# Optimization experiments

Hardware: AMD Instinct MI355X
Metric: run time of the kernel (lower is better)

## Reference

```python
import jax, jax.numpy as jnp
import numpy as np

D = 1024
H = 16
HD = D // H  # 64
FF = 4 * D
EPS = 1e-5

def _layernorm(x, g, b):
    mu = jnp.mean(x, axis=-1, keepdims=True)
    var = jnp.mean((x - mu) ** 2, axis=-1, keepdims=True)
    return (x - mu) * jax.lax.rsqrt(var + EPS) * g + b

def _apply_rotary(x, cos, sin):
    # x: [B,H,T,HD]; cos/sin: [T,HD//2] broadcast over B,H
    d = x.shape[-1] // 2
    x1, x2 = x[..., :d], x[..., d:]
    return jnp.concatenate([x1 * cos - x2 * sin, x2 * cos + x1 * sin], axis=-1)

def setup_inputs() -> dict:
    key = jax.random.key(0)
    ks = jax.random.split(key, 12)
    B, T = 4, 2048
    s = 0.02
    return {
        "x": jax.random.normal(ks[0], (B, T, D), jnp.float32),
        "rope_cos": jax.random.uniform(ks[1], (T, HD // 2), jnp.float32),
        "rope_sin": jax.random.uniform(ks[2], (T, HD // 2), jnp.float32),
        "ln1_g": jnp.ones((D,), jnp.float32),
        "ln1_b": jnp.zeros((D,), jnp.float32),
        "Wqkv": jax.random.normal(ks[3], (D, 3 * D), jnp.float32) * s,
        "bqkv": jnp.zeros((3 * D,), jnp.float32),
        "Wo": jax.random.normal(ks[4], (D, D), jnp.float32) * s,
        "bo": jnp.zeros((D,), jnp.float32),
        "ln2_g": jnp.ones((D,), jnp.float32),
        "ln2_b": jnp.zeros((D,), jnp.float32),
        "W1": jax.random.normal(ks[5], (D, FF), jnp.float32) * s,
        "b1": jnp.zeros((FF,), jnp.float32),
        "W2": jax.random.normal(ks[6], (FF, D), jnp.float32) * s,
        "b2": jnp.zeros((D,), jnp.float32),
    }

def reference(x, rope_cos, rope_sin, ln1_g, ln1_b, Wqkv, bqkv, Wo, bo, ln2_g, ln2_b, W1, b1, W2, b2):
    B, T, _ = x.shape
    h = _layernorm(x, ln1_g, ln1_b)
    qkv = (h @ Wqkv + bqkv).reshape(B, T, 3, H, HD)
    qkv = jnp.transpose(qkv, (2, 0, 3, 1, 4))  # [3,B,H,T,HD]
    q, k, v = qkv[0], qkv[1], qkv[2]
    q = _apply_rotary(q, rope_cos, rope_sin)
    k = _apply_rotary(k, rope_cos, rope_sin)
    scale = 1.0 / jnp.sqrt(jnp.float32(HD))
    scores = jnp.einsum('bhqd,bhkd->bhqk', q, k) * scale
    probs = jax.nn.softmax(scores, axis=-1)
    attn = jnp.einsum('bhqk,bhkd->bhqd', probs, v)
    attn = jnp.transpose(attn, (0, 2, 1, 3)).reshape(B, T, D)
    x = x + attn @ Wo + bo
    h2 = _layernorm(x, ln2_g, ln2_b)
    mlp = jax.nn.gelu(h2 @ W1 + b1, approximate=False) @ W2 + b2
    return x + mlp
```

## Files before the change

kernel.cpp:

```cpp
#include <hip/hip_runtime.h>
#include <hip/hip_bf16.h>
#include <math.h>

typedef __bf16 bf16x8 __attribute__((ext_vector_type(8)));
typedef float f32x4 __attribute__((ext_vector_type(4)));
typedef float f32x16 __attribute__((ext_vector_type(16)));
typedef unsigned short u16x8 __attribute__((ext_vector_type(8)));
typedef unsigned short u16x4 __attribute__((ext_vector_type(4)));
typedef unsigned int u32x4 __attribute__((ext_vector_type(4)));

#define DEV __device__ __forceinline__

DEV unsigned short f2bf(float f) { __bf16 h = (__bf16)f; return __builtin_bit_cast(unsigned short, h); }
DEV float bf2f(unsigned short u) { __bf16 h = __builtin_bit_cast(__bf16, u); return (float)h; }
DEV unsigned int pk2(float a, float b) {
  return (unsigned int)f2bf(a) | ((unsigned int)f2bf(b) << 16);
}

DEV void async_cp16(const void* g, void* l) {
  __builtin_amdgcn_global_load_lds((const __attribute__((address_space(1))) void*)g,
                                   (__attribute__((address_space(3))) void*)l, 16, 0, 0);
}

__global__ __launch_bounds__(256) void ln_kernel(const float* __restrict__ in,
    const float* __restrict__ g, const float* __restrict__ b,
    unsigned short* __restrict__ out)
{
  const int row = blockIdx.x;
  const int tid = threadIdx.x;
  const float4 v = ((const float4*)(in + (size_t)row * 1024))[tid];
  float s  = v.x + v.y + v.z + v.w;
  float sq = v.x*v.x + v.y*v.y + v.z*v.z + v.w*v.w;
  for (int m = 1; m < 64; m <<= 1) { s += __shfl_xor(s, m); sq += __shfl_xor(sq, m); }
  __shared__ float red[8];
  const int wave = tid >> 6;
  if ((tid & 63) == 0) { red[wave] = s; red[4 + wave] = sq; }
  __syncthreads();
  s  = red[0] + red[1] + red[2] + red[3];
  sq = red[4] + red[5] + red[6] + red[7];
  const float mu = s * (1.0f / 1024.0f);
  const float var = sq * (1.0f / 1024.0f) - mu * mu;
  const float rs = rsqrtf(var + 1e-5f);
  const float4 gv = ((const float4*)g)[tid];
  const float4 bv = ((const float4*)b)[tid];
  u16x4 o;
  o[0] = f2bf((v.x - mu) * rs * gv.x + bv.x);
  o[1] = f2bf((v.y - mu) * rs * gv.y + bv.y);
  o[2] = f2bf((v.z - mu) * rs * gv.z + bv.z);
  o[3] = f2bf((v.w - mu) * rs * gv.w + bv.w);
  *(u16x4*)(out + (size_t)row * 1024 + tid * 4) = o;
}

__global__ __launch_bounds__(256) void wtrans_kernel(const float* __restrict__ in,
    unsigned short* __restrict__ out, int K, int N)
{
  __shared__ float tile[32][33];
  const int n0 = blockIdx.x * 32, k0 = blockIdx.y * 32;
  const int r = threadIdx.x >> 5, c = threadIdx.x & 31;
  for (int p = 0; p < 4; ++p)
    tile[r + p * 8][c] = in[(size_t)(k0 + r + p * 8) * N + n0 + c];
  __syncthreads();
  for (int p = 0; p < 4; ++p)
    out[(size_t)(n0 + r + p * 8) * K + k0 + c] = f2bf(tile[c][r + p * 8]);
}

enum { EPI_QKV = 0, EPI_ATTNO = 1, EPI_GELU = 2, EPI_FINAL = 3 };

template <int EPI>
__global__ __launch_bounds__(256, 3) void gemm_bt(
    const unsigned short* __restrict__ A,
    const unsigned short* __restrict__ Bt,
    const float* __restrict__ bias,
    const float* __restrict__ resid,
    void* __restrict__ out,
    int M, int N, int K,
    const float* __restrict__ rc, const float* __restrict__ rsn,
    unsigned short* __restrict__ vout)
{
  __shared__ unsigned short lA[4096] __attribute__((aligned(16)));
  __shared__ unsigned short lB[4096] __attribute__((aligned(16)));
  const int tid = threadIdx.x;
  const int lane = tid & 63, wave = tid >> 6;
  const int l15 = lane & 15, quad = lane >> 4;
  const int bm = blockIdx.y * 128, bn = blockIdx.x * 128;
  const int wm = (wave & 1) * 64, wn = (wave >> 1) * 64;

  const unsigned short* ga[2]; const unsigned short* gb[2];
  unsigned short* la_dst[2]; unsigned short* lb_dst[2];
  for (int it = 0; it < 2; ++it) {
    const int s = it * 256 + tid;
    const int gg = s >> 3;
    const int v = (s & 7) ^ (gg & 7);
    const int row = gg * 2 + (v >> 2);
    const int ch = v & 3;
    ga[it] = A  + (size_t)(bm + row) * K + ch * 8;
    gb[it] = Bt + (size_t)(bn + row) * K + ch * 8;
    const int base = (it * 256 + wave * 64) * 8;
    la_dst[it] = lA + base;
    lb_dst[it] = lB + base;
  }
  int offA[4], offB[4];
  for (int i = 0; i < 4; ++i) {
    int row = wm + i * 16 + l15;
    int gg = row >> 1;
    int si = (((row & 1) << 2) | quad) ^ (gg & 7);
    offA[i] = ((gg << 3) | si) * 8;
    row = wn + i * 16 + l15;
    gg = row >> 1;
    si = (((row & 1) << 2) | quad) ^ (gg & 7);
    offB[i] = ((gg << 3) | si) * 8;
  }

  f32x4 acc[4][4];
  for (int i = 0; i < 4; ++i)
    for (int j = 0; j < 4; ++j)
      acc[i][j] = f32x4{0.f, 0.f, 0.f, 0.f};

  for (int k0 = 0; k0 < K; k0 += 32) {
    async_cp16(ga[0], la_dst[0]);
    async_cp16(ga[1], la_dst[1]);
    async_cp16(gb[0], lb_dst[0]);
    async_cp16(gb[1], lb_dst[1]);
    ga[0] += 32; ga[1] += 32; gb[0] += 32; gb[1] += 32;
    __syncthreads();
    bf16x8 af[4], bfr[4];
    for (int i = 0; i < 4; ++i) af[i]  = *(const bf16x8*)(lA + offA[i]);
    for (int j = 0; j < 4; ++j) bfr[j] = *(const bf16x8*)(lB + offB[j]);
    for (int i = 0; i < 4; ++i)
      for (int j = 0; j < 4; ++j)
        acc[i][j] = __builtin_amdgcn_mfma_f32_16x16x32_bf16(af[i], bfr[j], acc[i][j], 0, 0, 0);
    __syncthreads();
  }

  float bvals[4];
  for (int j = 0; j < 4; ++j) bvals[j] = bias[bn + wn + j * 16 + l15];

  if constexpr (EPI == EPI_QKV) {
    const int cn = bn + wn;
    const int sec = cn >> 10;
    if (sec == 2) {
      const int b = bm >> 11;
      const int hh = (cn & 1023) >> 6;
      for (int i = 0; i < 4; ++i) {
        const int t0 = (bm + wm + i * 16 + quad * 4) & 2047;
        for (int j = 0; j < 4; ++j) {
          const int d = j * 16 + l15;
          u16x4 o;
          for (int r = 0; r < 4; ++r) o[r] = f2bf(acc[i][j][r] + bvals[j]);
          *(u16x4*)(vout + ((size_t)((b * 16 + hh) * 64 + d)) * 2048 + t0) = o;
        }
      }
    } else {
      const float qscale = (sec == 0) ? 0.18033688f : 1.0f;
      unsigned short* qkvout = (unsigned short*)out;
      for (int i = 0; i < 4; ++i) {
        for (int r = 0; r < 4; ++r) {
          const int row = bm + wm + i * 16 + quad * 4 + r;
          const int t = row & 2047;
          for (int j = 0; j < 2; ++j) {
            const int d = j * 16 + l15;
            const float v1 = acc[i][j][r] + bvals[j];
            const float v2 = acc[i][j + 2][r] + bvals[j + 2];
            const float c = rc[t * 32 + d], s = rsn[t * 32 + d];
            const float o1 = (v1 * c - v2 * s) * qscale;
            const float o2 = (v2 * c + v1 * s) * qscale;
            const size_t base = (size_t)row * 3072 + cn + d;
            qkvout[base] = f2bf(o1);
            qkvout[base + 32] = f2bf(o2);
          }
        }
      }
    }
  } else {
    for (int i = 0; i < 4; ++i) {
      for (int r = 0; r < 4; ++r) {
        const size_t row = bm + wm + i * 16 + quad * 4 + r;
        for (int j = 0; j < 4; ++j) {
          const size_t col = bn + wn + j * 16 + l15;
          const float v = acc[i][j][r] + bvals[j];
          const size_t idx = row * (size_t)N + col;
          if constexpr (EPI == EPI_ATTNO) {
            ((float*)out)[idx] = resid[idx] + v;
          } else if constexpr (EPI == EPI_GELU) {
            const float gl = 0.5f * v * (1.0f + erff(v * 0.70710678118f));
            ((unsigned short*)out)[idx] = f2bf(gl);
          } else {
            ((float*)out)[idx] = resid[idx] + v;
          }
        }
      }
    }
  }
}

__global__ __launch_bounds__(256, 4) void attn_kernel(
    const unsigned short* __restrict__ qkv,
    const unsigned short* __restrict__ vt,
    unsigned short* __restrict__ outb)
{
  __shared__ unsigned short Ks[2][4096] __attribute__((aligned(16)));
  __shared__ unsigned short Vs[2][4096] __attribute__((aligned(16)));
  __shared__ float Sred[128];

  const int tid = threadIdx.x;
  const int lane = tid & 63, wave = tid >> 6;
  const int l31 = lane & 31, hl = lane >> 5;
  const int bh = blockIdx.y, b = bh >> 4, h = bh & 15;
  const int q0 = blockIdx.x * 64;
  const int qsub = (wave & 1) * 32;
  const int ksub = (wave >> 1) * 32;

  bf16x8 qf[4];
  {
    const unsigned short* qp = qkv + (size_t)(b * 2048 + q0 + qsub + l31) * 3072 + h * 64 + hl * 8;
    for (int kc = 0; kc < 4; ++kc) qf[kc] = *(const bf16x8*)(qp + kc * 16);
  }

  const int s0 = wave * 128 + lane, s1 = s0 + 64;
  const int r0 = s0 >> 3, c0 = (lane & 7) ^ (r0 & 7);
  const int r1 = s1 >> 3, c1 = (lane & 7) ^ (r1 & 7);
  const unsigned short* kbase = qkv + (size_t)(b * 2048) * 3072 + 1024 + h * 64;
  const unsigned short* ks0 = kbase + (size_t)r0 * 3072 + c0 * 8;
  const unsigned short* ks1 = kbase + (size_t)r1 * 3072 + c1 * 8;
  const unsigned short* vbase = vt + (size_t)bh * 64 * 2048;
  const unsigned short* vs0 = vbase + (size_t)r0 * 2048 + c0 * 8;
  const unsigned short* vs1 = vbase + (size_t)r1 * 2048 + c1 * 8;
  unsigned short* kd[2] = { Ks[0] + wave * 1024, Ks[1] + wave * 1024 };
  unsigned short* vd[2] = { Vs[0] + wave * 1024, Vs[1] + wave * 1024 };

  int offK[4], offV[2][2];
  for (int kc = 0; kc < 4; ++kc) {
    const int rk = ksub + l31;
    offK[kc] = (rk * 8 + ((2 * kc + hl) ^ (rk & 7))) * 8;
  }
  for (int dn = 0; dn < 2; ++dn)
    for (int c = 0; c < 2; ++c) {
      const int rv = dn * 32 + l31;
      const int ch = (ksub >> 3) + 2 * c + hl;
      offV[dn][c] = (rv * 8 + (ch ^ (rv & 7))) * 8;
    }

  f32x16 accO[2];
  for (int dn = 0; dn < 2; ++dn)
    for (int i = 0; i < 16; ++i) accO[dn][i] = 0.f;
  float rsum = 0.f;

  async_cp16(ks0, kd[0]);
  async_cp16(ks1, kd[0] + 512);
  async_cp16(vs0, vd[0]);
  async_cp16(vs1, vd[0] + 512);

  for (int kt = 0; kt < 32; ++kt) {
    const int cur = kt & 1, nxt = cur ^ 1;
    __syncthreads();
    if (kt < 31) {
      const size_t ko = (size_t)(kt + 1) * 64 * 3072;
      const int vo = (kt + 1) * 64;
      async_cp16(ks0 + ko, kd[nxt]);
      async_cp16(ks1 + ko, kd[nxt] + 512);
      async_cp16(vs0 + vo, vd[nxt]);
      async_cp16(vs1 + vo, vd[nxt] + 512);
    }
    f32x16 accS;
    for (int i = 0; i < 16; ++i) accS[i] = 0.f;
    for (int kc = 0; kc < 4; ++kc) {
      const bf16x8 kf = *(const bf16x8*)(Ks[cur] + offK[kc]);
      accS = __builtin_amdgcn_mfma_f32_32x32x16_bf16(kf, qf[kc], accS, 0, 0, 0);
    }
    float p[16];
    for (int i = 0; i < 16; ++i) {
      p[i] = __builtin_amdgcn_exp2f(accS[i]);
      rsum += p[i];
    }

    for (int c = 0; c < 2; ++c) {
      const unsigned int xlo0 = pk2(p[8 * c + 0], p[8 * c + 1]);
      const unsigned int xlo1 = pk2(p[8 * c + 2], p[8 * c + 3]);
      const unsigned int xhi0 = pk2(p[8 * c + 4], p[8 * c + 5]);
      const unsigned int xhi1 = pk2(p[8 * c + 6], p[8 * c + 7]);
      const unsigned int recv0 = __shfl_xor((int)(hl ? xlo0 : xhi0), 32);
      const unsigned int recv1 = __shfl_xor((int)(hl ? xlo1 : xhi1), 32);
      u32x4 w;
      w[0] = hl ? recv0 : xlo0;
      w[1] = hl ? recv1 : xlo1;
      w[2] = hl ? xhi0 : recv0;
      w[3] = hl ? xhi1 : recv1;
      const bf16x8 pf = __builtin_bit_cast(bf16x8, w);
      for (int dn = 0; dn < 2; ++dn) {
        const bf16x8 vf = *(const bf16x8*)(Vs[cur] + offV[dn][c]);
        accO[dn] = __builtin_amdgcn_mfma_f32_32x32x16_bf16(pf, vf, accO[dn], 0, 0, 0);
      }
    }
  }

  __syncthreads();
  float* Obuf = (float*)&Ks[0][0];

  {
    const float rs2 = rsum + __shfl_xor(rsum, 32);
    if (hl == 0) Sred[(wave >> 1) * 64 + qsub + l31] = rs2;
  }
  if (ksub == 0) {
    for (int dn = 0; dn < 2; ++dn)
      for (int reg = 0; reg < 16; ++reg) {
        const int rq = qsub + (reg & 3) + 8 * (reg >> 2) + 4 * hl;
        Obuf[rq * 64 + dn * 32 + l31] = accO[dn][reg];
      }
  }
  __syncthreads();
  if (ksub == 32) {
    for (int reg = 0; reg < 16; ++reg) {
      const int rq = qsub + (reg & 3) + 8 * (reg >> 2) + 4 * hl;
      const float inv = 1.0f / (Sred[rq] + Sred[64 + rq]);
      const size_t row = (size_t)(b * 2048 + q0 + rq);
      for (int dn = 0; dn < 2; ++dn) {
        const float o = (Obuf[rq * 64 + dn * 32 + l31] + accO[dn][reg]) * inv;
        outb[row * 1024 + h * 64 + dn * 32 + l31] = f2bf(o);
      }
    }
  }
}

extern "C" void kernel_launch(void* const* d_in, const int* in_sizes, int n_in,
                              void* d_out, int out_size, void* d_ws, size_t ws_size,
                              hipStream_t stream)
{
  const float* x        = (const float*)d_in[0];
  const float* rope_cos = (const float*)d_in[1];
  const float* rope_sin = (const float*)d_in[2];
  const float* ln1_g    = (const float*)d_in[3];
  const float* ln1_b    = (const float*)d_in[4];
  const float* Wqkv     = (const float*)d_in[5];
  const float* bqkv     = (const float*)d_in[6];
  const float* Wo       = (const float*)d_in[7];
  const float* bo       = (const float*)d_in[8];
  const float* ln2_g    = (const float*)d_in[9];
  const float* ln2_b    = (const float*)d_in[10];
  const float* W1       = (const float*)d_in[11];
  const float* b1       = (const float*)d_in[12];
  const float* W2       = (const float*)d_in[13];
  const float* b2       = (const float*)d_in[14];
  float* outp = (float*)d_out;

  char* ws = (char*)d_ws;
  size_t off = 0;
  auto alloc = [&](size_t bytes) -> void* {
    void* p = ws + off;
    off += (bytes + 255) & ~(size_t)255;
    return p;
  };
  unsigned short* h1    = (unsigned short*)alloc(8192ull * 1024 * 2);
  unsigned short* wqkvT = (unsigned short*)alloc(3072ull * 1024 * 2);
  unsigned short* woT   = (unsigned short*)alloc(1024ull * 1024 * 2);
  unsigned short* w1T   = (unsigned short*)alloc(4096ull * 1024 * 2);
  unsigned short* w2T   = (unsigned short*)alloc(1024ull * 4096 * 2);
  unsigned short* qkv   = (unsigned short*)alloc(8192ull * 3072 * 2);
  unsigned short* vtb   = (unsigned short*)alloc(64ull * 64 * 2048 * 2);
  unsigned short* h2    = (unsigned short*)alloc(8192ull * 1024 * 2);
  unsigned short* ffb   = (unsigned short*)alloc(8192ull * 4096 * 2);

  wtrans_kernel<<<dim3(96, 32), 256, 0, stream>>>(Wqkv, wqkvT, 1024, 3072);
  wtrans_kernel<<<dim3(32, 32), 256, 0, stream>>>(Wo, woT, 1024, 1024);
  wtrans_kernel<<<dim3(128, 32), 256, 0, stream>>>(W1, w1T, 1024, 4096);
  wtrans_kernel<<<dim3(32, 128), 256, 0, stream>>>(W2, w2T, 4096, 1024);

  ln_kernel<<<8192, 256, 0, stream>>>(x, ln1_g, ln1_b, h1);
  gemm_bt<EPI_QKV><<<dim3(24, 64), 256, 0, stream>>>(h1, wqkvT, bqkv, nullptr, qkv,
                                                     8192, 3072, 1024, rope_cos, rope_sin, vtb);
  attn_kernel<<<dim3(32, 64), 256, 0, stream>>>(qkv, vtb, h1);
  gemm_bt<EPI_ATTNO><<<dim3(8, 64), 256, 0, stream>>>(h1, woT, bo, x, d_out,
                                                      8192, 1024, 1024, nullptr, nullptr, nullptr);
  ln_kernel<<<8192, 256, 0, stream>>>(outp, ln2_g, ln2_b, h2);
  gemm_bt<EPI_GELU><<<dim3(32, 64), 256, 0, stream>>>(h2, w1T, b1, nullptr, ffb,
                                                      8192, 4096, 1024, nullptr, nullptr, nullptr);
  gemm_bt<EPI_FINAL><<<dim3(8, 64), 256, 0, stream>>>(ffb, w2T, b2, outp, d_out,
                                                      8192, 1024, 4096, nullptr, nullptr, nullptr);
}
```

Measured before the change: 577.9 us.

## Deepen GEMM K-tile to 64 and give each attention wave its own query rows

The GEMM kernel now stages a 64-wide K slice per iteration with a simpler per-row XOR swizzle, halving the number of barrier pairs per K loop at the cost of doubling LDS per block. The attention kernel switches from splitting keys across wave pairs to having each of four waves own 32 query rows and process all 64 keys per tile. This removes the cross-wave partial-output reduction through LDS and doubles K/V tile reuse per block, but it halves the grid size and raises per-wave work, which may reduce occupancy and parallelism.

Result: faster. 522.3 us (-9.6%).

```diff
diff --git a/kernel.cpp b/kernel.cpp
--- a/kernel.cpp
+++ b/kernel.cpp
@@ -77,58 +77,53 @@
     const float* __restrict__ rc, const float* __restrict__ rsn,
     unsigned short* __restrict__ vout)
 {
-  __shared__ unsigned short lA[4096] __attribute__((aligned(16)));
-  __shared__ unsigned short lB[4096] __attribute__((aligned(16)));
+  __shared__ unsigned short lA[8192] __attribute__((aligned(16)));
+  __shared__ unsigned short lB[8192] __attribute__((aligned(16)));
   const int tid = threadIdx.x;
   const int lane = tid & 63, wave = tid >> 6;
   const int l15 = lane & 15, quad = lane >> 4;
   const int bm = blockIdx.y * 128, bn = blockIdx.x * 128;
   const int wm = (wave & 1) * 64, wn = (wave >> 1) * 64;
 
-  const unsigned short* ga[2]; const unsigned short* gb[2];
-  unsigned short* la_dst[2]; unsigned short* lb_dst[2];
-  for (int it = 0; it < 2; ++it) {
+  const unsigned short* ga[4]; const unsigned short* gb[4];
+  unsigned short* la_dst[4]; unsigned short* lb_dst[4];
+  for (int it = 0; it < 4; ++it) {
     const int s = it * 256 + tid;
-    const int gg = s >> 3;
-    const int v = (s & 7) ^ (gg & 7);
-    const int row = gg * 2 + (v >> 2);
-    const int ch = v & 3;
+    const int row = s >> 3;
+    const int ch = (s & 7) ^ (row & 7);
     ga[it] = A  + (size_t)(bm + row) * K + ch * 8;
     gb[it] = Bt + (size_t)(bn + row) * K + ch * 8;
     const int base = (it * 256 + wave * 64) * 8;
     la_dst[it] = lA + base;
     lb_dst[it] = lB + base;
   }
-  int offA[4], offB[4];
-  for (int i = 0; i < 4; ++i) {
-    int row = wm + i * 16 + l15;
-    int gg = row >> 1;
-    int si = (((row & 1) << 2) | quad) ^ (gg & 7);
-    offA[i] = ((gg << 3) | si) * 8;
-    row = wn + i * 16 + l15;
-    gg = row >> 1;
-    si = (((row & 1) << 2) | quad) ^ (gg & 7);
-    offB[i] = ((gg << 3) | si) * 8;
-  }
+  int offA[2][4], offB[2][4];
+  for (int ks = 0; ks < 2; ++ks)
+    for (int i = 0; i < 4; ++i) {
+      int row = wm + i * 16 + l15;
+      offA[ks][i] = (row * 8 + ((ks * 4 + quad) ^ (row & 7))) * 8;
+      row = wn + i * 16 + l15;
+      offB[ks][i] = (row * 8 + ((ks * 4 + quad) ^ (row & 7))) * 8;
+    }
 
   f32x4 acc[4][4];
   for (int i = 0; i < 4; ++i)
     for (int j = 0; j < 4; ++j)
       acc[i][j] = f32x4{0.f, 0.f, 0.f, 0.f};
 
-  for (int k0 = 0; k0 < K; k0 += 32) {
-    async_cp16(ga[0], la_dst[0]);
-    async_cp16(ga[1], la_dst[1]);
-    async_cp16(gb[0], lb_dst[0]);
-    async_cp16(gb[1], lb_dst[1]);
-    ga[0] += 32; ga[1] += 32; gb[0] += 32; gb[1] += 32;
+  for (int k0 = 0; k0 < K; k0 += 64) {
+    for (int it = 0; it < 4; ++it) async_cp16(ga[it], la_dst[it]);
+    for (int it = 0; it < 4; ++it) async_cp16(gb[it], lb_dst[it]);
+    for (int it = 0; it < 4; ++it) { ga[it] += 64; gb[it] += 64; }
     __syncthreads();
-    bf16x8 af[4], bfr[4];
-    for (int i = 0; i < 4; ++i) af[i]  = *(const bf16x8*)(lA + offA[i]);
-    for (int j = 0; j < 4; ++j) bfr[j] = *(const bf16x8*)(lB + offB[j]);
-    for (int i = 0; i < 4; ++i)
-      for (int j = 0; j < 4; ++j)
-        acc[i][j] = __builtin_amdgcn_mfma_f32_16x16x32_bf16(af[i], bfr[j], acc[i][j], 0, 0, 0);
+    for (int ks = 0; ks < 2; ++ks) {
+      bf16x8 af[4], bfr[4];
+      for (int i = 0; i < 4; ++i) af[i]  = *(const bf16x8*)(lA + offA[ks][i]);
+      for (int j = 0; j < 4; ++j) bfr[j] = *(const bf16x8*)(lB + offB[ks][j]);
+      for (int i = 0; i < 4; ++i)
+        for (int j = 0; j < 4; ++j)
+          acc[i][j] = __builtin_amdgcn_mfma_f32_16x16x32_bf16(af[i], bfr[j], acc[i][j], 0, 0, 0);
+    }
     __syncthreads();
   }
 
@@ -206,9 +201,8 @@
   const int lane = tid & 63, wave = tid >> 6;
   const int l31 = lane & 31, hl = lane >> 5;
   const int bh = blockIdx.y, b = bh >> 4, h = bh & 15;
-  const int q0 = blockIdx.x * 64;
-  const int qsub = (wave & 1) * 32;
-  const int ksub = (wave >> 1) * 32;
+  const int q0 = blockIdx.x * 128;
+  const int qsub = wave * 32;
 
   bf16x8 qf[4];
   {
@@ -228,16 +222,16 @@
   unsigned short* kd[2] = { Ks[0] + wave * 1024, Ks[1] + wave * 1024 };
   unsigned short* vd[2] = { Vs[0] + wave * 1024, Vs[1] + wave * 1024 };
 
-  int offK[4], offV[2][2];
-  for (int kc = 0; kc < 4; ++kc) {
-    const int rk = ksub + l31;
-    offK[kc] = (rk * 8 + ((2 * kc + hl) ^ (rk & 7))) * 8;
-  }
+  int offK[2][4], offV[2][4];
+  for (int g = 0; g < 2; ++g)
+    for (int kc = 0; kc < 4; ++kc) {
+      const int rk = g * 32 + l31;
+      offK[g][kc] = (rk * 8 + ((2 * kc + hl) ^ (rk & 7))) * 8;
+    }
   for (int dn = 0; dn < 2; ++dn)
-    for (int c = 0; c < 2; ++c) {
+    for (int t = 0; t < 4; ++t) {
       const int rv = dn * 32 + l31;
-      const int ch = (ksub >> 3) + 2 * c + hl;
-      offV[dn][c] = (rv * 8 + (ch ^ (rv & 7))) * 8;
+      offV[dn][t] = (rv * 8 + ((2 * t + hl) ^ (rv & 7))) * 8;
     }
 
   f32x16 accO[2];
@@ -261,63 +255,51 @@
       async_cp16(vs0 + vo, vd[nxt]);
       async_cp16(vs1 + vo, vd[nxt] + 512);
     }
-    f32x16 accS;
-    for (int i = 0; i < 16; ++i) accS[i] = 0.f;
-    for (int kc = 0; kc < 4; ++kc) {
-      const bf16x8 kf = *(const bf16x8*)(Ks[cur] + offK[kc]);
-      accS = __builtin_amdgcn_mfma_f32_32x32x16_bf16(kf, qf[kc], accS, 0, 0, 0);
-    }
-    float p[16];
-    for (int i = 0; i < 16; ++i) {
-      p[i] = __builtin_amdgcn_exp2f(accS[i]);
-      rsum += p[i];
-    }
-
-    for (int c = 0; c < 2; ++c) {
-      const unsigned int xlo0 = pk2(p[8 * c + 0], p[8 * c + 1]);
-      const unsigned int xlo1 = pk2(p[8 * c + 2], p[8 * c + 3]);
-      const unsigned int xhi0 = pk2(p[8 * c + 4], p[8 * c + 5]);
-      const unsigned int xhi1 = pk2(p[8 * c + 6], p[8 * c + 7]);
-      const unsigned int recv0 = __shfl_xor((int)(hl ? xlo0 : xhi0), 32);
-      const unsigned int recv1 = __shfl_xor((int)(hl ? xlo1 : xhi1), 32);
-      u32x4 w;
-      w[0] = hl ? recv0 : xlo0;
-      w[1] = hl ? recv1 : xlo1;
-      w[2] = hl ? xhi0 : recv0;
-      w[3] = hl ? xhi1 : recv1;
-      const bf16x8 pf = __builtin_bit_cast(bf16x8, w);
-      for (int dn = 0; dn < 2; ++dn) {
-        const bf16x8 vf = *(const bf16x8*)(Vs[cur] + offV[dn][c]);
-        accO[dn] = __builtin_amdgcn_mfma_f32_32x32x16_bf16(pf, vf, accO[dn], 0, 0, 0);
-      }
-    }
-  }
-
-  __syncthreads();
-  float* Obuf = (float*)&Ks[0][0];
+    for (int g = 0; g < 2; ++g) {
+      f32x16 accS;
+      for (int i = 0; i < 16; ++i) accS[i] = 0.f;
+      for (int kc = 0; kc < 4; ++kc) {
+        const bf16x8 kf = *(const bf16x8*)(Ks[cur] + offK[g][kc]);
+        accS = __builtin_amdgcn_mfma_f32_32x32x16_bf16(kf, qf[kc], accS, 0, 0, 0);
+      }
+      float p[16];
+      for (int i = 0; i < 16; ++i) {
+        p[i] = __builtin_amdgcn_exp2f(accS[i]);
+        rsum += p[i];
+      }
+      for (int c = 0; c < 2; ++c) {
+        const unsigned int xlo0 = pk2(p[8 * c + 0], p[8 * c + 1]);
+        const unsigned int xlo1 = pk2(p[8 * c + 2], p[8 * c + 3]);
+        const unsigned int xhi0 = pk2(p[8 * c + 4], p[8 * c + 5]);
+        const unsigned int xhi1 = pk2(p[8 * c + 6], p[8 * c + 7]);
+        const unsigned int recv0 = __shfl_xor((int)(hl ? xlo0 : xhi0), 32);
+        const unsigned int recv1 = __shfl_xor((int)(hl ? xlo1 : xhi1), 32);
+        u32x4 w;
+        w[0] = hl ? recv0 : xlo0;
+        w[1] = hl ? recv1 : xlo1;
+        w[2] = hl ? xhi0 : recv0;
+        w[3] = hl ? xhi1 : recv1;
+        const bf16x8 pf = __builtin_bit_cast(bf16x8, w);
+        const int t = 2 * g + c;
+        for (int dn = 0; dn < 2; ++dn) {
+          const bf16x8 vf = *(const bf16x8*)(Vs[cur] + offV[dn][t]);
+          accO[dn] = __builtin_amdgcn_mfma_f32_32x32x16_bf16(pf, vf, accO[dn], 0, 0, 0);
+        }
+      }
+    }
+  }
 
   {
     const float rs2 = rsum + __shfl_xor(rsum, 32);
-    if (hl == 0) Sred[(wave >> 1) * 64 + qsub + l31] = rs2;
-  }
-  if (ksub == 0) {
+    if (hl == 0) Sred[qsub + l31] = rs2;
+  }
+  __syncthreads();
+  for (int reg = 0; reg < 16; ++reg) {
+    const int rq = qsub + (reg & 3) + 8 * (reg >> 2) + 4 * hl;
+    const float inv = 1.0f / Sred[rq];
+    const size_t row = (size_t)(b * 2048 + q0 + rq);
     for (int dn = 0; dn < 2; ++dn)
-      for (int reg = 0; reg < 16; ++reg) {
-        const int rq = qsub + (reg & 3) + 8 * (reg >> 2) + 4 * hl;
-        Obuf[rq * 64 + dn * 32 + l31] = accO[dn][reg];
-      }
-  }
-  __syncthreads();
-  if (ksub == 32) {
-    for (int reg = 0; reg < 16; ++reg) {
-      const int rq = qsub + (reg & 3) + 8 * (reg >> 2) + 4 * hl;
-      const float inv = 1.0f / (Sred[rq] + Sred[64 + rq]);
-      const size_t row = (size_t)(b * 2048 + q0 + rq);
-      for (int dn = 0; dn < 2; ++dn) {
-        const float o = (Obuf[rq * 64 + dn * 32 + l31] + accO[dn][reg]) * inv;
-        outb[row * 1024 + h * 64 + dn * 32 + l31] = f2bf(o);
-      }
-    }
+      outb[row * 1024 + h * 64 + dn * 32 + l31] = f2bf(accO[dn][reg] * inv);
   }
 }
 
@@ -367,7 +349,7 @@
   ln_kernel<<<8192, 256, 0, stream>>>(x, ln1_g, ln1_b, h1);
   gemm_bt<EPI_QKV><<<dim3(24, 64), 256, 0, stream>>>(h1, wqkvT, bqkv, nullptr, qkv,
                                                      8192, 3072, 1024, rope_cos, rope_sin, vtb);
-  attn_kernel<<<dim3(32, 64), 256, 0, stream>>>(qkv, vtb, h1);
+  attn_kernel<<<dim3(16, 64), 256, 0, stream>>>(qkv, vtb, h1);
   gemm_bt<EPI_ATTNO><<<dim3(8, 64), 256, 0, stream>>>(h1, woT, bo, x, d_out,
                                                       8192, 1024, 1024, nullptr, nullptr, nullptr);
   ln_kernel<<<8192, 256, 0, stream>>>(outp, ln2_g, ln2_b, h2);
```
